# Optimization experiments

Hardware: AMD Instinct MI355X
Metric: run time of the kernel (lower is better)

## Reference

```python
import jax, jax.numpy as jnp
import numpy as np
import math

D = 768
H = 12
DH = D // H
L = 2
EPS = 1e-12
NEG = -10000.0


def layer_norm(x, w, b):
    u = jnp.mean(x, axis=-1, keepdims=True)
    s = jnp.mean((x - u) ** 2, axis=-1, keepdims=True)
    return w * ((x - u) / jnp.sqrt(s + EPS)) + b


def mha(q_in, k_in, v_in, mask, qw, qb, kw, kb, vw, vb):
    # q_in: (B,Lq,D); k_in/v_in: (B,Lk,D); mask: (B,Lq,Lk) or (B,1,Lk)
    B, Lq, _ = q_in.shape
    def proj(x, w, b):
        y = x @ w.T + b
        return y.reshape(x.shape[0], x.shape[1], H, DH).transpose(0, 2, 1, 3)
    q = proj(q_in, qw, qb)  # (B,H,Lq,DH)
    k = proj(k_in, kw, kb)
    v = proj(v_in, vw, vb)
    scores = jnp.einsum('bhqd,bhkd->bhqk', q, k) / math.sqrt(DH)
    scores = scores + (1.0 - mask[:, None]) * NEG  # additive mask, (B,1,Lq,Lk) broadcast
    probs = jax.nn.softmax(scores, axis=-1)
    ctx = jnp.einsum('bhqk,bhkd->bhqd', probs, v)
    return ctx.transpose(0, 2, 1, 3).reshape(B, Lq, D)


def setup_inputs() -> dict:
    key = jax.random.key(0)
    ks = jax.random.split(key, 8)
    B, Lt, Lv = 8, 1024, 512
    inp = {
        'dec_hidden_states': jax.random.normal(ks[0], (B, Lt, D), jnp.float32),
        'dec_mask': jnp.ones((B, Lt), jnp.float32),
        'enc_outputs': jax.random.normal(ks[1], (B, Lv, D), jnp.float32),
        'enc_mask': jnp.ones((B, Lv), jnp.float32),
    }
    wkeys = jax.random.split(ks[2], 7)
    names = ['sa_qw', 'sa_kw', 'sa_vw', 'ca_qw', 'ca_kw', 'ca_vw', 'out_w']
    for n, k in zip(names, wkeys):
        inp[n] = 0.02 * jax.random.normal(k, (L, D, D), jnp.float32)
    for n in ['sa_qb', 'sa_kb', 'sa_vb', 'ca_qb', 'ca_kb', 'ca_vb', 'out_b', 'n1_b', 'n2_b', 'n3_b']:
        inp[n] = jnp.zeros((L, D), jnp.float32)
    for n in ['n1_w', 'n2_w', 'n3_w']:
        inp[n] = jnp.ones((L, D), jnp.float32)
    return inp


def reference(dec_hidden_states, dec_mask, enc_outputs, enc_mask,
              sa_qw, sa_qb, sa_kw, sa_kb, sa_vw, sa_vb, n1_w, n1_b,
              ca_qw, ca_qb, ca_kw, ca_kb, ca_vw, ca_vb, n2_w, n2_b,
              out_w, out_b, n3_w, n3_b):
    Lt = dec_hidden_states.shape[1]
    causal = jnp.tril(jnp.ones((Lt, Lt), dec_mask.dtype))
    self_mask = dec_mask[:, None, :] * causal[None]        # (B,Lt,Lt)
    cross_mask = enc_mask[:, None, :]                      # (B,1,Lv)

    params = (sa_qw, sa_qb, sa_kw, sa_kb, sa_vw, sa_vb, n1_w, n1_b,
              ca_qw, ca_qb, ca_kw, ca_kb, ca_vw, ca_vb, n2_w, n2_b,
              out_w, out_b, n3_w, n3_b)

    def body(x, p):
        (qw, qb, kw, kb, vw, vb, w1, b1,
         cqw, cqb, ckw, ckb, cvw, cvb, w2, b2,
         ow, ob, w3, b3) = p
        a = mha(x, x, x, self_mask, qw, qb, kw, kb, vw, vb)
        x1 = layer_norm(a + x, w1, b1)
        c = mha(x1, enc_outputs, enc_outputs, cross_mask, cqw, cqb, ckw, ckb, cvw, cvb)
        x2 = layer_norm(x1 + c, w2, b2)
        # BertOutput called with (x2, x2): LN(dense(x2) + x2)
        y = layer_norm(x2 @ ow.T + ob + x2, w3, b3)
        return y, None

    out, _ = jax.lax.scan(body, dec_hidden_states, params)
    return out
```

## Files before the change

### kernel.cpp

```cpp
#include <hip/hip_runtime.h>
#include <hip/hip_bf16.h>

#define DMODEL 768
#define NH 12
#define DH 64
#define NEGC -10000.0f

#define AS1 __attribute__((address_space(1)))
#define AS3 __attribute__((address_space(3)))

typedef __bf16 bf16_t;
typedef __bf16 bf16x8 __attribute__((ext_vector_type(8)));
typedef float f32x4 __attribute__((ext_vector_type(4)));

__device__ __forceinline__ f32x4 mfma16(bf16x8 a, bf16x8 b, f32x4 c) {
    return __builtin_amdgcn_mfma_f32_16x16x32_bf16(a, b, c, 0, 0, 0);
}

__device__ __forceinline__ void gl_lds16(const bf16_t* g, void* l) {
    __builtin_amdgcn_global_load_lds((const AS1 void*)g, (AS3 void*)l, 16, 0, 0);
}

__global__ void probe_kernel(const unsigned int* m, int* flag) {
    *flag = (m[0] == 0x3F803F80u) ? 1 : 0;
}

__device__ __forceinline__ void cvt_group(const void* src, bf16_t* dst, int g, int isbf16) {
    if (isbf16) {
        ((bf16x8*)dst)[g] = ((const bf16x8*)src)[g];
    } else {
        const float* s = (const float*)src + (size_t)g * 8;
        bf16x8 v;
#pragma unroll
        for (int i = 0; i < 8; i++) v[i] = (bf16_t)s[i];
        ((bf16x8*)dst)[g] = v;
    }
}

__global__ __launch_bounds__(256) void cvt_kernel(const void* src, bf16_t* dst,
                                                  const int* flag, int n) {
    int g = blockIdx.x * 256 + threadIdx.x;
    if (g * 8 >= n) return;
    cvt_group(src, dst, g, *flag);
}

__global__ __launch_bounds__(256) void cvt7_kernel(
    const void* s0, const void* s1, const void* s2, const void* s3,
    const void* s4, const void* s5, const void* s6,
    bf16_t* dst, const int* flag)
{
    const void* srcs[7] = {s0, s1, s2, s3, s4, s5, s6};
    const void* src = srcs[blockIdx.y];
    bf16_t* d = dst + (size_t)blockIdx.y * 1179648;
    int g = blockIdx.x * 256 + threadIdx.x;
    cvt_group(src, d, g, *flag);
}

__global__ __launch_bounds__(256) void cvt13_kernel(
    const void* s0, const void* s1, const void* s2, const void* s3,
    const void* s4, const void* s5, const void* s6, const void* s7,
    const void* s8, const void* s9, const void* s10, const void* s11,
    const void* s12, bf16_t* dst, const int* flag)
{
    const void* srcs[13] = {s0, s1, s2, s3, s4, s5, s6, s7, s8, s9, s10, s11, s12};
    const void* src = srcs[blockIdx.x];
    bf16_t* d = dst + (size_t)blockIdx.x * 1536;
    int g = threadIdx.x;
    if (g >= 192) return;
    cvt_group(src, d, g, *flag);
}

__global__ __launch_bounds__(256) void gemm128_kernel(
    const bf16_t* __restrict__ X,
    const bf16_t* __restrict__ W0, const bf16_t* __restrict__ W1,
    const bf16_t* __restrict__ W2,
    const bf16_t* __restrict__ B0, const bf16_t* __restrict__ B1,
    const bf16_t* __restrict__ B2,
    bf16_t* __restrict__ O0, bf16_t* __restrict__ O1, bf16_t* __restrict__ O2,
    int nx, int ny, int nz, int vz, int lkShift)
{
    __shared__ __attribute__((aligned(16))) bf16_t alds[2][128 * 64];
    __shared__ __attribute__((aligned(16))) bf16_t blds[2][128 * 64];

    const int tid  = threadIdx.x;
    const int lane = tid & 63;
    const int w    = tid >> 6;
    const int r    = lane & 15;
    const int q4   = lane >> 4;

    const int id     = blockIdx.x;
    const int xcd    = id & 7;
    const int slot   = id >> 3;
    const int planes = nx * nz;
    const int band   = xcd + 8 * (slot / planes);
    const int p      = slot % planes;
    const int z      = p / nx;
    const int bx     = p - z * nx;
    const int row0   = band * 128;
    const int col0   = bx * 128;
    const int wrow   = (w >> 1) * 64;
    const int wcol   = (w & 1) * 64;

    const bf16_t* W    = (z == 0) ? W0 : ((z == 1) ? W1 : W2);
    const bf16_t* bias = (z == 0) ? B0 : ((z == 1) ? B1 : B2);
    bf16_t*       out  = (z == 0) ? O0 : ((z == 1) ? O1 : O2);
    const int     mode = (z == vz) ? 1 : 0;

    const f32x4 zero4 = {0.f, 0.f, 0.f, 0.f};
    f32x4 acc[4][4];
#pragma unroll
    for (int i = 0; i < 4; i++)
#pragma unroll
        for (int j = 0; j < 4; j++) acc[i][j] = zero4;

    const int srow = (w * 256 + lane) >> 3;
    const int sgc  = (lane & 7) ^ (srow & 7);
    const bf16_t* Xs = X + (size_t)(row0 + srow) * DMODEL + sgc * 8;
    const bf16_t* Ws = W + (size_t)(col0 + srow) * DMODEL + sgc * 8;

    auto stage = [&](int buf, int kb) {
#pragma unroll
        for (int j = 0; j < 4; j++) {
            gl_lds16(Xs + (size_t)(j * 8) * DMODEL + kb,
                     (char*)&alds[buf][0] + w * 4096 + j * 1024);
            gl_lds16(Ws + (size_t)(j * 8) * DMODEL + kb,
                     (char*)&blds[buf][0] + w * 4096 + j * 1024);
        }
    };

    const int NIT = DMODEL / 64;
    stage(0, 0);
    for (int i = 0; i < NIT; i++) {
        const int cur = i & 1;
        asm volatile("s_waitcnt lgkmcnt(0)" ::: "memory");
        __builtin_amdgcn_s_barrier();
        if (i + 1 < NIT) {
            stage(cur ^ 1, (i + 1) * 64);
            asm volatile("s_waitcnt vmcnt(8)" ::: "memory");
        } else {
            asm volatile("s_waitcnt vmcnt(0)" ::: "memory");
        }
        __builtin_amdgcn_s_barrier();

        const bf16_t* al = alds[cur];
        const bf16_t* bl = blds[cur];
#pragma unroll
        for (int ks = 0; ks < 2; ks++) {
            bf16x8 af[4], bf[4];
#pragma unroll
            for (int ii = 0; ii < 4; ii++) {
                int rr_ = wrow + ii * 16 + r;
                int pc  = (ks * 4 + q4) ^ (rr_ & 7);
                af[ii] = *(const bf16x8*)&al[rr_ * 64 + pc * 8];
            }
#pragma unroll
            for (int j = 0; j < 4; j++) {
                int cc_ = wcol + j * 16 + r;
                int pc  = (ks * 4 + q4) ^ (cc_ & 7);
                bf[j] = *(const bf16x8*)&bl[cc_ * 64 + pc * 8];
            }
#pragma unroll
            for (int ii = 0; ii < 4; ii++)
#pragma unroll
                for (int j = 0; j < 4; j++)
                    acc[ii][j] = mfma16(af[ii], bf[j], acc[ii][j]);
        }
    }

#pragma unroll
    for (int i = 0; i < 4; i++)
#pragma unroll
        for (int j = 0; j < 4; j++)
#pragma unroll
            for (int rr = 0; rr < 4; rr++) {
                int grow = row0 + wrow + i * 16 + q4 * 4 + rr;
                int gcol = col0 + wcol + j * 16 + r;
                float v = acc[i][j][rr] + (float)bias[gcol];
                if (mode == 0) {
                    out[(size_t)grow * DMODEL + gcol] = (bf16_t)v;
                } else {
                    int bidx = grow >> lkShift;
                    int t    = grow & ((1 << lkShift) - 1);
                    int h    = gcol >> 6;
                    int dd   = gcol & 63;
                    out[((size_t)((bidx * NH + h) * 64 + dd) << lkShift) + t] = (bf16_t)v;
                }
            }
}

__global__ __launch_bounds__(256) void attn_kernel(
    const bf16_t* Q, const bf16_t* __restrict__ K,
    const bf16_t* __restrict__ Vt, const bf16_t* __restrict__ mask,
    bf16_t* ctx, int Lq, int Lk, int causal)
{
    __shared__ __attribute__((aligned(16))) bf16_t kvlds[2][2][4096];
    __shared__ __attribute__((aligned(16))) bf16_t plds[4][1024];
    const int tid  = threadIdx.x;
    const int lane = tid & 63;
    const int wv   = tid >> 6;
    const int r    = lane & 15;
    const int q4   = lane >> 4;
    const int b    = blockIdx.z;
    const int h    = blockIdx.y;
    const int qblk = (gridDim.x - 1 - blockIdx.x) * 64;
    const int qbase = qblk + wv * 16;

    const bf16_t* Qp = Q + ((size_t)(b * Lq + qbase + r)) * DMODEL + h * DH + q4 * 8;
    bf16x8 qf0 = *(const bf16x8*)(Qp);
    bf16x8 qf1 = *(const bf16x8*)(Qp + 32);
    const bf16_t* Kg = K + ((size_t)b * Lk) * DMODEL + h * DH;
    const bf16_t* Vg = Vt + ((size_t)(b * NH + h) * DH) * Lk;
    const bf16_t* mp = mask + (size_t)b * Lk;

    const f32x4 zero4 = {0.f, 0.f, 0.f, 0.f};
    float psum[4] = {0.f, 0.f, 0.f, 0.f};
    f32x4 o[4] = {zero4, zero4, zero4, zero4};

    const int nt = causal ? ((qblk >> 6) + 1) : (Lk >> 6);

    auto stage = [&](int buf, int kb) {
#pragma unroll
        for (int j = 0; j < 2; j++) {
            gl_lds16(Kg + (size_t)(kb + wv * 16 + r) * DMODEL + (j * 4 + q4) * 8,
                     &kvlds[buf][0][wv * 1024 + j * 512]);
            gl_lds16(Vg + (size_t)(wv * 16 + r) * Lk + kb + (j * 4 + q4) * 8,
                     &kvlds[buf][1][wv * 1024 + j * 512]);
        }
    };

    stage(0, 0);
    for (int i = 0; i < nt; i++) {
        const int kb  = i << 6;
        const int cur = i & 1;
        asm volatile("s_waitcnt lgkmcnt(0)" ::: "memory");
        __builtin_amdgcn_s_barrier();
        float mb[4];
#pragma unroll
        for (int t = 0; t < 4; t++)
            mb[t] = (1.f - (float)mp[kb + t * 16 + r]) * NEGC;
        if (i + 1 < nt) {
            stage(cur ^ 1, kb + 64);
            asm volatile("s_waitcnt vmcnt(4)" ::: "memory");
        } else {
            asm volatile("s_waitcnt vmcnt(0)" ::: "memory");
        }
        __builtin_amdgcn_s_barrier();

        const bf16_t* kl = kvlds[cur][0];
        const bf16_t* vl = kvlds[cur][1];
        f32x4 s[4];
#pragma unroll
        for (int t = 0; t < 4; t++) {
            bf16x8 k0 = *(const bf16x8*)&kl[t * 1024 + lane * 8];
            bf16x8 k1 = *(const bf16x8*)&kl[t * 1024 + 512 + lane * 8];
            s[t] = mfma16(qf1, k1, mfma16(qf0, k0, zero4));
        }
#pragma unroll
        for (int t = 0; t < 4; t++) {
#pragma unroll
            for (int rr = 0; rr < 4; rr++) {
                float f = s[t][rr] * 0.125f + mb[t];
                float pv = __expf(f);
                if (causal && kb + t * 16 + r > qbase + q4 * 4 + rr) pv = 0.f;
                psum[rr] += pv;
                plds[wv][(t * 2 + (r >> 3)) * 128 + (q4 * 4 + rr) * 8 + (r & 7)] =
                    (bf16_t)pv;
            }
        }
        bf16x8 pa0 = *(const bf16x8*)&plds[wv][lane * 8];
        bf16x8 pa1 = *(const bf16x8*)&plds[wv][512 + lane * 8];
#pragma unroll
        for (int nc = 0; nc < 4; nc++) {
            bf16x8 v0 = *(const bf16x8*)&vl[nc * 1024 + lane * 8];
            bf16x8 v1 = *(const bf16x8*)&vl[nc * 1024 + 512 + lane * 8];
            o[nc] = mfma16(pa1, v1, mfma16(pa0, v0, o[nc]));
        }
    }

#pragma unroll
    for (int rr = 0; rr < 4; rr++) {
        psum[rr] += __shfl_xor(psum[rr], 1, 64);
        psum[rr] += __shfl_xor(psum[rr], 2, 64);
        psum[rr] += __shfl_xor(psum[rr], 4, 64);
        psum[rr] += __shfl_xor(psum[rr], 8, 64);
    }
#pragma unroll
    for (int nc = 0; nc < 4; nc++)
#pragma unroll
        for (int rr = 0; rr < 4; rr++) {
            int qi = qbase + q4 * 4 + rr;
            ctx[((size_t)(b * Lq + qi)) * DMODEL + h * DH + nc * 16 + r] =
                (bf16_t)(o[nc][rr] / psum[rr]);
        }
}

__global__ __launch_bounds__(256) void ln_kernel(
    const bf16_t* a, const bf16_t* res,
    const bf16_t* __restrict__ w, const bf16_t* __restrict__ b,
    void* out, int fin, const int* __restrict__ flag)
{
    __shared__ float red[8];
    const int row = blockIdx.x;
    const int tid = threadIdx.x;
    const int lane = tid & 63;
    const int wv = tid >> 6;
    const bf16_t* ap = a + (size_t)row * DMODEL;
    const bf16_t* rp = res + (size_t)row * DMODEL;
    const int outf32 = fin && (*flag == 0);

    float v[3];
#pragma unroll
    for (int i = 0; i < 3; i++) {
        int c = tid + i * 256;
        v[i] = (float)ap[c] + (float)rp[c];
    }
    float s = v[0] + v[1] + v[2];
#pragma unroll
    for (int m = 1; m < 64; m <<= 1) s += __shfl_xor(s, m, 64);
    if (lane == 0) red[wv] = s;
    __syncthreads();
    float u = (red[0] + red[1] + red[2] + red[3]) * (1.0f / DMODEL);
    float d0 = v[0] - u, d1 = v[1] - u, d2 = v[2] - u;
    float s2 = d0 * d0 + d1 * d1 + d2 * d2;
#pragma unroll
    for (int m = 1; m < 64; m <<= 1) s2 += __shfl_xor(s2, m, 64);
    if (lane == 0) red[4 + wv] = s2;
    __syncthreads();
    float var = (red[4] + red[5] + red[6] + red[7]) * (1.0f / DMODEL);
    float rstd = rsqrtf(var + 1e-12f);
#pragma unroll
    for (int i = 0; i < 3; i++) {
        int c = tid + i * 256;
        float y = ((v[i] - u) * rstd) * (float)w[c] + (float)b[c];
        if (outf32) ((float*)out)[(size_t)row * DMODEL + c] = y;
        else        ((bf16_t*)out)[(size_t)row * DMODEL + c] = (bf16_t)y;
    }
}

extern "C" void kernel_launch(void* const* d_in, const int* in_sizes, int n_in,
                              void* d_out, int out_size, void* d_ws, size_t ws_size,
                              hipStream_t stream)
{
    const int B = 8, Lt = 1024, Lv = 512;
    const size_t A = (size_t)B * Lt * DMODEL;
    const size_t E = (size_t)B * Lv * DMODEL;
    const size_t WT = 2 * (size_t)DMODEL * DMODEL;
    const int WSZ = DMODEL * DMODEL;

    char* p = (char*)d_ws;
    int* flagp = (int*)p;            p += 64;
    bf16_t* cdec = (bf16_t*)p;       p += A * 2;
    bf16_t* cenc = (bf16_t*)p;       p += E * 2;
    bf16_t* cdm  = (bf16_t*)p;       p += (size_t)B * Lt * 2;
    bf16_t* cem  = (bf16_t*)p;       p += (size_t)B * Lv * 2;
    bf16_t* cw   = (bf16_t*)p;       p += 7 * WT * 2;
    bf16_t* cb   = (bf16_t*)p;       p += 13 * 1536 * 2;
    bf16_t* b0   = (bf16_t*)p;       p += A * 2;
    bf16_t* b1   = (bf16_t*)p;       p += A * 2;
    bf16_t* b2   = (bf16_t*)p;       p += A * 2;
    bf16_t* dob  = (bf16_t*)d_out;

    const bf16_t* sa_qw = cw + 0 * WT, * sa_kw = cw + 1 * WT, * sa_vw = cw + 2 * WT;
    const bf16_t* ca_qw = cw + 3 * WT, * ca_kw = cw + 4 * WT, * ca_vw = cw + 5 * WT;
    const bf16_t* out_w = cw + 6 * WT;
    const bf16_t* sa_qb = cb + 0 * 1536, * sa_kb = cb + 1 * 1536, * sa_vb = cb + 2 * 1536;
    const bf16_t* ca_qb = cb + 3 * 1536, * ca_kb = cb + 4 * 1536, * ca_vb = cb + 5 * 1536;
    const bf16_t* out_b = cb + 6 * 1536;
    const bf16_t* n1_b  = cb + 7 * 1536, * n2_b = cb + 8 * 1536, * n3_b = cb + 9 * 1536;
    const bf16_t* n1_w  = cb + 10 * 1536, * n2_w = cb + 11 * 1536, * n3_w = cb + 12 * 1536;

    probe_kernel<<<1, 1, 0, stream>>>((const unsigned int*)d_in[1], flagp);
    cvt_kernel<<<dim3((unsigned)(A / 2048)), 256, 0, stream>>>(d_in[0], cdec, flagp, (int)A);
    cvt_kernel<<<dim3((unsigned)(E / 2048)), 256, 0, stream>>>(d_in[2], cenc, flagp, (int)E);
    cvt_kernel<<<dim3(4),  256, 0, stream>>>(d_in[1], cdm, flagp, B * Lt);
    cvt_kernel<<<dim3(2),  256, 0, stream>>>(d_in[3], cem, flagp, B * Lv);
    cvt7_kernel<<<dim3(576, 7), 256, 0, stream>>>(
        d_in[4], d_in[5], d_in[6], d_in[7], d_in[8], d_in[9], d_in[10], cw, flagp);
    cvt13_kernel<<<dim3(13), 256, 0, stream>>>(
        d_in[11], d_in[12], d_in[13], d_in[14], d_in[15], d_in[16], d_in[17],
        d_in[18], d_in[19], d_in[20], d_in[21], d_in[22], d_in[23], cb, flagp);

    const int Mdec = B * Lt;
    const int Menc = B * Lv;
    dim3 blk(256);
    dim3 gQKV(6 * 64 * 3);
    dim3 gOne(6 * 64 * 1);
    dim3 gKVe(6 * 32 * 2);
    dim3 gAttn(Lt / 64, NH, B);
    dim3 gLN(Mdec);

    for (int l = 0; l < 2; l++) {
        const bf16_t* xin = (l == 0) ? cdec : dob;
        gemm128_kernel<<<gQKV, blk, 0, stream>>>(
            xin, sa_qw + l * WSZ, sa_kw + l * WSZ, sa_vw + l * WSZ,
            sa_qb + l * DMODEL, sa_kb + l * DMODEL, sa_vb + l * DMODEL,
            b0, b1, b2, 6, 64, 3, 2, 10);
        attn_kernel<<<gAttn, blk, 0, stream>>>(b0, b1, b2, cdm, b0, Lt, Lt, 1);
        ln_kernel<<<gLN, blk, 0, stream>>>(b0, xin, n1_w + l * DMODEL, n1_b + l * DMODEL, b0, 0, flagp);
        gemm128_kernel<<<gOne, blk, 0, stream>>>(
            b0, ca_qw + l * WSZ, ca_qw, ca_qw,
            ca_qb + l * DMODEL, ca_qb, ca_qb,
            b1, b1, b1, 6, 64, 1, -1, 0);
        gemm128_kernel<<<gKVe, blk, 0, stream>>>(
            cenc, ca_kw + l * WSZ, ca_vw + l * WSZ, ca_vw,
            ca_kb + l * DMODEL, ca_vb + l * DMODEL, ca_vb,
            b2, dob, dob, 6, 32, 2, 1, 9);
        attn_kernel<<<gAttn, blk, 0, stream>>>(b1, b2, dob, cem, b1, Lt, Lv, 0);
        ln_kernel<<<gLN, blk, 0, stream>>>(b1, b0, n2_w + l * DMODEL, n2_b + l * DMODEL, b1, 0, flagp);
        gemm128_kernel<<<gOne, blk, 0, stream>>>(
            b1, out_w + l * WSZ, out_w, out_w,
            out_b + l * DMODEL, out_b, out_b,
            b2, b2, b2, 6, 64, 1, -1, 0);
        ln_kernel<<<gLN, blk, 0, stream>>>(b2, b1, n3_w + l * DMODEL, n3_b + l * DMODEL, dob, (l == 1) ? 1 : 0, flagp);
    }
}
```

Before: 702.7 us.

## Halve GEMM K-tile to raise occupancy and merge cross-attn Q/KV launches

The GEMM's LDS K-tile drops from 64 to 32, halving shared memory per block, and launch bounds now request 4 blocks per CU to increase occupancy. The swizzle and staging are adjusted to match, and the loop runs twice as many iterations. The GEMM now takes a separate input pointer and row-band count per z-plane, so the cross-attention Q projection (decoder rows) and the K/V projections (encoder rows) run in one launch, with excess blocks exiting early. This cuts one launch and lets the smaller GEMMs share the device, at the cost of more barriers per K step and idle early-exit blocks.

Result: no change. 697.7 us (-0.7%).

```diff
diff --git a/kernel.cpp b/kernel.cpp
--- a/kernel.cpp
+++ b/kernel.cpp
@@ -70,17 +70,18 @@
     cvt_group(src, d, g, *flag);
 }
 
-__global__ __launch_bounds__(256) void gemm128_kernel(
-    const bf16_t* __restrict__ X,
+__global__ __launch_bounds__(256, 4) void gemm128_kernel(
+    const bf16_t* __restrict__ X0, const bf16_t* __restrict__ X1,
+    const bf16_t* __restrict__ X2,
     const bf16_t* __restrict__ W0, const bf16_t* __restrict__ W1,
     const bf16_t* __restrict__ W2,
     const bf16_t* __restrict__ B0, const bf16_t* __restrict__ B1,
     const bf16_t* __restrict__ B2,
     bf16_t* __restrict__ O0, bf16_t* __restrict__ O1, bf16_t* __restrict__ O2,
-    int nx, int ny, int nz, int vz, int lkShift)
-{
-    __shared__ __attribute__((aligned(16))) bf16_t alds[2][128 * 64];
-    __shared__ __attribute__((aligned(16))) bf16_t blds[2][128 * 64];
+    int nx, int ny0, int ny1, int ny2, int nz, int vz, int lkShift)
+{
+    __shared__ __attribute__((aligned(16))) bf16_t alds[2][128 * 32];
+    __shared__ __attribute__((aligned(16))) bf16_t blds[2][128 * 32];
 
     const int tid  = threadIdx.x;
     const int lane = tid & 63;
@@ -96,11 +97,16 @@
     const int p      = slot % planes;
     const int z      = p / nx;
     const int bx     = p - z * nx;
+
+    const int nyz = (z == 0) ? ny0 : ((z == 1) ? ny1 : ny2);
+    if (band >= nyz) return;
+
     const int row0   = band * 128;
     const int col0   = bx * 128;
     const int wrow   = (w >> 1) * 64;
     const int wcol   = (w & 1) * 64;
 
+    const bf16_t* X    = (z == 0) ? X0 : ((z == 1) ? X1 : X2);
     const bf16_t* W    = (z == 0) ? W0 : ((z == 1) ? W1 : W2);
     const bf16_t* bias = (z == 0) ? B0 : ((z == 1) ? B1 : B2);
     bf16_t*       out  = (z == 0) ? O0 : ((z == 1) ? O1 : O2);
@@ -113,30 +119,30 @@
 #pragma unroll
         for (int j = 0; j < 4; j++) acc[i][j] = zero4;
 
-    const int srow = (w * 256 + lane) >> 3;
-    const int sgc  = (lane & 7) ^ (srow & 7);
+    const int srow = w * 32 + (lane >> 2);
+    const int sgc  = (lane & 3) ^ (srow & 3);
     const bf16_t* Xs = X + (size_t)(row0 + srow) * DMODEL + sgc * 8;
     const bf16_t* Ws = W + (size_t)(col0 + srow) * DMODEL + sgc * 8;
 
     auto stage = [&](int buf, int kb) {
 #pragma unroll
-        for (int j = 0; j < 4; j++) {
-            gl_lds16(Xs + (size_t)(j * 8) * DMODEL + kb,
-                     (char*)&alds[buf][0] + w * 4096 + j * 1024);
-            gl_lds16(Ws + (size_t)(j * 8) * DMODEL + kb,
-                     (char*)&blds[buf][0] + w * 4096 + j * 1024);
+        for (int j = 0; j < 2; j++) {
+            gl_lds16(Xs + (size_t)(j * 16) * DMODEL + kb,
+                     (char*)&alds[buf][0] + w * 2048 + j * 1024);
+            gl_lds16(Ws + (size_t)(j * 16) * DMODEL + kb,
+                     (char*)&blds[buf][0] + w * 2048 + j * 1024);
         }
     };
 
-    const int NIT = DMODEL / 64;
+    const int NIT = DMODEL / 32;
     stage(0, 0);
     for (int i = 0; i < NIT; i++) {
         const int cur = i & 1;
         asm volatile("s_waitcnt lgkmcnt(0)" ::: "memory");
         __builtin_amdgcn_s_barrier();
         if (i + 1 < NIT) {
-            stage(cur ^ 1, (i + 1) * 64);
-            asm volatile("s_waitcnt vmcnt(8)" ::: "memory");
+            stage(cur ^ 1, (i + 1) * 32);
+            asm volatile("s_waitcnt vmcnt(4)" ::: "memory");
         } else {
             asm volatile("s_waitcnt vmcnt(0)" ::: "memory");
         }
@@ -144,27 +150,24 @@
 
         const bf16_t* al = alds[cur];
         const bf16_t* bl = blds[cur];
-#pragma unroll
-        for (int ks = 0; ks < 2; ks++) {
-            bf16x8 af[4], bf[4];
-#pragma unroll
-            for (int ii = 0; ii < 4; ii++) {
-                int rr_ = wrow + ii * 16 + r;
-                int pc  = (ks * 4 + q4) ^ (rr_ & 7);
-                af[ii] = *(const bf16x8*)&al[rr_ * 64 + pc * 8];
-            }
-#pragma unroll
-            for (int j = 0; j < 4; j++) {
-                int cc_ = wcol + j * 16 + r;
-                int pc  = (ks * 4 + q4) ^ (cc_ & 7);
-                bf[j] = *(const bf16x8*)&bl[cc_ * 64 + pc * 8];
-            }
-#pragma unroll
-            for (int ii = 0; ii < 4; ii++)
-#pragma unroll
-                for (int j = 0; j < 4; j++)
-                    acc[ii][j] = mfma16(af[ii], bf[j], acc[ii][j]);
-        }
+        bf16x8 af[4], bf[4];
+#pragma unroll
+        for (int ii = 0; ii < 4; ii++) {
+            int rr_ = wrow + ii * 16 + r;
+            int pc  = q4 ^ (rr_ & 3);
+            af[ii] = *(const bf16x8*)&al[rr_ * 32 + pc * 8];
+        }
+#pragma unroll
+        for (int j = 0; j < 4; j++) {
+            int cc_ = wcol + j * 16 + r;
+            int pc  = q4 ^ (cc_ & 3);
+            bf[j] = *(const bf16x8*)&bl[cc_ * 32 + pc * 8];
+        }
+#pragma unroll
+        for (int ii = 0; ii < 4; ii++)
+#pragma unroll
+            for (int j = 0; j < 4; j++)
+                acc[ii][j] = mfma16(af[ii], bf[j], acc[ii][j]);
     }
 
 #pragma unroll
@@ -380,37 +383,34 @@
         d_in[11], d_in[12], d_in[13], d_in[14], d_in[15], d_in[16], d_in[17],
         d_in[18], d_in[19], d_in[20], d_in[21], d_in[22], d_in[23], cb, flagp);
 
-    const int Mdec = B * Lt;
-    const int Menc = B * Lv;
     dim3 blk(256);
     dim3 gQKV(6 * 64 * 3);
+    dim3 gCrs(6 * 64 * 3);
     dim3 gOne(6 * 64 * 1);
-    dim3 gKVe(6 * 32 * 2);
     dim3 gAttn(Lt / 64, NH, B);
-    dim3 gLN(Mdec);
+    dim3 gLN(B * Lt);
 
     for (int l = 0; l < 2; l++) {
         const bf16_t* xin = (l == 0) ? cdec : dob;
         gemm128_kernel<<<gQKV, blk, 0, stream>>>(
-            xin, sa_qw + l * WSZ, sa_kw + l * WSZ, sa_vw + l * WSZ,
+            xin, xin, xin,
+            sa_qw + l * WSZ, sa_kw + l * WSZ, sa_vw + l * WSZ,
             sa_qb + l * DMODEL, sa_kb + l * DMODEL, sa_vb + l * DMODEL,
-            b0, b1, b2, 6, 64, 3, 2, 10);
+            b0, b1, b2, 6, 64, 64, 64, 3, 2, 10);
         attn_kernel<<<gAttn, blk, 0, stream>>>(b0, b1, b2, cdm, b0, Lt, Lt, 1);
         ln_kernel<<<gLN, blk, 0, stream>>>(b0, xin, n1_w + l * DMODEL, n1_b + l * DMODEL, b0, 0, flagp);
-        gemm128_kernel<<<gOne, blk, 0, stream>>>(
-            b0, ca_qw + l * WSZ, ca_qw, ca_qw,
-            ca_qb + l * DMODEL, ca_qb, ca_qb,
-            b1, b1, b1, 6, 64, 1, -1, 0);
-        gemm128_kernel<<<gKVe, blk, 0, stream>>>(
-            cenc, ca_kw + l * WSZ, ca_vw + l * WSZ, ca_vw,
-            ca_kb + l * DMODEL, ca_vb + l * DMODEL, ca_vb,
-            b2, dob, dob, 6, 32, 2, 1, 9);
+        gemm128_kernel<<<gCrs, blk, 0, stream>>>(
+            b0, cenc, cenc,
+            ca_qw + l * WSZ, ca_kw + l * WSZ, ca_vw + l * WSZ,
+            ca_qb + l * DMODEL, ca_kb + l * DMODEL, ca_vb + l * DMODEL,
+            b1, b2, dob, 6, 64, 32, 32, 3, 2, 9);
         attn_kernel<<<gAttn, blk, 0, stream>>>(b1, b2, dob, cem, b1, Lt, Lv, 0);
         ln_kernel<<<gLN, blk, 0, stream>>>(b1, b0, n2_w + l * DMODEL, n2_b + l * DMODEL, b1, 0, flagp);
         gemm128_kernel<<<gOne, blk, 0, stream>>>(
-            b1, out_w + l * WSZ, out_w, out_w,
+            b1, b1, b1,
+            out_w + l * WSZ, out_w, out_w,
             out_b + l * DMODEL, out_b, out_b,
-            b2, b2, b2, 6, 64, 1, -1, 0);
+            b2, b2, b2, 6, 64, 64, 64, 1, -1, 0);
         ln_kernel<<<gLN, blk, 0, stream>>>(b2, b1, n3_w + l * DMODEL, n3_b + l * DMODEL, dob, (l == 1) ? 1 : 0, flagp);
     }
 }
```

## Use 256x256-tile GEMM for QKV projections and merge cross-attention Q/KV launches

Applied to the files above, without the earlier changes.

Adds a 512-thread GEMM kernel with 256x256 output tiles and per-plane input pointers, used for the self-attention QKV projection and the cross-attention projections. The cross-attention Q projection (from decoder states) and K/V projections (from encoder outputs) now run in one launch, with bands beyond each plane's row count exiting early. The transposed V output is written as packed 4-element vector stores. Larger tiles raise operand reuse and cut launches, but the grid shrinks to 288 blocks with large LDS use, which risks partial-wave imbalance and lower occupancy on the device.

New measurement: 672.8 us. -4.3%, faster.

```diff
diff --git a/kernel.cpp b/kernel.cpp
--- a/kernel.cpp
+++ b/kernel.cpp
@@ -12,6 +12,7 @@
 typedef __bf16 bf16_t;
 typedef __bf16 bf16x8 __attribute__((ext_vector_type(8)));
 typedef float f32x4 __attribute__((ext_vector_type(4)));
+typedef unsigned int u32x2 __attribute__((ext_vector_type(2)));
 
 __device__ __forceinline__ f32x4 mfma16(bf16x8 a, bf16x8 b, f32x4 c) {
     return __builtin_amdgcn_mfma_f32_16x16x32_bf16(a, b, c, 0, 0, 0);
@@ -70,17 +71,18 @@
     cvt_group(src, d, g, *flag);
 }
 
-__global__ __launch_bounds__(256) void gemm128_kernel(
-    const bf16_t* __restrict__ X,
+__global__ __launch_bounds__(512, 2) void gemm256_kernel(
+    const bf16_t* __restrict__ X0, const bf16_t* __restrict__ X1,
+    const bf16_t* __restrict__ X2,
     const bf16_t* __restrict__ W0, const bf16_t* __restrict__ W1,
     const bf16_t* __restrict__ W2,
     const bf16_t* __restrict__ B0, const bf16_t* __restrict__ B1,
     const bf16_t* __restrict__ B2,
     bf16_t* __restrict__ O0, bf16_t* __restrict__ O1, bf16_t* __restrict__ O2,
-    int nx, int ny, int nz, int vz, int lkShift)
-{
-    __shared__ __attribute__((aligned(16))) bf16_t alds[2][128 * 64];
-    __shared__ __attribute__((aligned(16))) bf16_t blds[2][128 * 64];
+    int nx, int ny0, int ny1, int ny2, int nz, int vz, int lkShift)
+{
+    __shared__ __attribute__((aligned(16))) bf16_t alds[2][256 * 64];
+    __shared__ __attribute__((aligned(16))) bf16_t blds[2][256 * 64];
 
     const int tid  = threadIdx.x;
     const int lane = tid & 63;
@@ -96,24 +98,31 @@
     const int p      = slot % planes;
     const int z      = p / nx;
     const int bx     = p - z * nx;
-    const int row0   = band * 128;
-    const int col0   = bx * 128;
-    const int wrow   = (w >> 1) * 64;
-    const int wcol   = (w & 1) * 64;
-
+
+    const int nyz = (z == 0) ? ny0 : ((z == 1) ? ny1 : ny2);
+    if (band >= nyz) return;
+
+    const int row0 = band * 256;
+    const int col0 = bx * 256;
+    const int wr   = w >> 2;
+    const int wc   = w & 3;
+    const int wrow = wr * 128;
+    const int wcol = wc * 64;
+
+    const bf16_t* X    = (z == 0) ? X0 : ((z == 1) ? X1 : X2);
     const bf16_t* W    = (z == 0) ? W0 : ((z == 1) ? W1 : W2);
     const bf16_t* bias = (z == 0) ? B0 : ((z == 1) ? B1 : B2);
     bf16_t*       out  = (z == 0) ? O0 : ((z == 1) ? O1 : O2);
     const int     mode = (z == vz) ? 1 : 0;
 
     const f32x4 zero4 = {0.f, 0.f, 0.f, 0.f};
-    f32x4 acc[4][4];
-#pragma unroll
-    for (int i = 0; i < 4; i++)
+    f32x4 acc[8][4];
+#pragma unroll
+    for (int i = 0; i < 8; i++)
 #pragma unroll
         for (int j = 0; j < 4; j++) acc[i][j] = zero4;
 
-    const int srow = (w * 256 + lane) >> 3;
+    const int srow = w * 32 + (lane >> 3);
     const int sgc  = (lane & 7) ^ (srow & 7);
     const bf16_t* Xs = X + (size_t)(row0 + srow) * DMODEL + sgc * 8;
     const bf16_t* Ws = W + (size_t)(col0 + srow) * DMODEL + sgc * 8;
@@ -146,6 +155,121 @@
         const bf16_t* bl = blds[cur];
 #pragma unroll
         for (int ks = 0; ks < 2; ks++) {
+            bf16x8 af[8], bf[4];
+#pragma unroll
+            for (int ii = 0; ii < 8; ii++) {
+                int rr_ = wrow + ii * 16 + r;
+                int pc  = (ks * 4 + q4) ^ (rr_ & 7);
+                af[ii] = *(const bf16x8*)&al[rr_ * 64 + pc * 8];
+            }
+#pragma unroll
+            for (int j = 0; j < 4; j++) {
+                int cc_ = wcol + j * 16 + r;
+                int pc  = (ks * 4 + q4) ^ (cc_ & 7);
+                bf[j] = *(const bf16x8*)&bl[cc_ * 64 + pc * 8];
+            }
+#pragma unroll
+            for (int ii = 0; ii < 8; ii++)
+#pragma unroll
+                for (int j = 0; j < 4; j++)
+                    acc[ii][j] = mfma16(af[ii], bf[j], acc[ii][j]);
+        }
+    }
+
+#pragma unroll
+    for (int i = 0; i < 8; i++)
+#pragma unroll
+        for (int j = 0; j < 4; j++) {
+            int gcol = col0 + wcol + j * 16 + r;
+            float bv = (float)bias[gcol];
+            if (mode == 0) {
+#pragma unroll
+                for (int rr = 0; rr < 4; rr++) {
+                    int grow = row0 + wrow + i * 16 + q4 * 4 + rr;
+                    out[(size_t)grow * DMODEL + gcol] = (bf16_t)(acc[i][j][rr] + bv);
+                }
+            } else {
+                int growb = row0 + wrow + i * 16 + q4 * 4;
+                int bidx  = growb >> lkShift;
+                int t     = growb & ((1 << lkShift) - 1);
+                int h     = gcol >> 6;
+                int dd    = gcol & 63;
+                union { bf16_t h4[4]; u32x2 v; } pk;
+#pragma unroll
+                for (int rr = 0; rr < 4; rr++)
+                    pk.h4[rr] = (bf16_t)(acc[i][j][rr] + bv);
+                *reinterpret_cast<u32x2*>(
+                    &out[((size_t)((bidx * NH + h) * 64 + dd) << lkShift) + t]) = pk.v;
+            }
+        }
+}
+
+__global__ __launch_bounds__(256) void gemm128_kernel(
+    const bf16_t* __restrict__ X,
+    const bf16_t* __restrict__ W,
+    const bf16_t* __restrict__ Bb,
+    bf16_t* __restrict__ out,
+    int nx, int ny)
+{
+    __shared__ __attribute__((aligned(16))) bf16_t alds[2][128 * 64];
+    __shared__ __attribute__((aligned(16))) bf16_t blds[2][128 * 64];
+
+    const int tid  = threadIdx.x;
+    const int lane = tid & 63;
+    const int w    = tid >> 6;
+    const int r    = lane & 15;
+    const int q4   = lane >> 4;
+
+    const int id     = blockIdx.x;
+    const int xcd    = id & 7;
+    const int slot   = id >> 3;
+    const int band   = xcd + 8 * (slot / nx);
+    const int bx     = slot % nx;
+    const int row0   = band * 128;
+    const int col0   = bx * 128;
+    const int wrow   = (w >> 1) * 64;
+    const int wcol   = (w & 1) * 64;
+
+    const f32x4 zero4 = {0.f, 0.f, 0.f, 0.f};
+    f32x4 acc[4][4];
+#pragma unroll
+    for (int i = 0; i < 4; i++)
+#pragma unroll
+        for (int j = 0; j < 4; j++) acc[i][j] = zero4;
+
+    const int srow = w * 32 + (lane >> 3);
+    const int sgc  = (lane & 7) ^ (srow & 7);
+    const bf16_t* Xs = X + (size_t)(row0 + srow) * DMODEL + sgc * 8;
+    const bf16_t* Ws = W + (size_t)(col0 + srow) * DMODEL + sgc * 8;
+
+    auto stage = [&](int buf, int kb) {
+#pragma unroll
+        for (int j = 0; j < 4; j++) {
+            gl_lds16(Xs + (size_t)(j * 8) * DMODEL + kb,
+                     (char*)&alds[buf][0] + w * 4096 + j * 1024);
+            gl_lds16(Ws + (size_t)(j * 8) * DMODEL + kb,
+                     (char*)&blds[buf][0] + w * 4096 + j * 1024);
+        }
+    };
+
+    const int NIT = DMODEL / 64;
+    stage(0, 0);
+    for (int i = 0; i < NIT; i++) {
+        const int cur = i & 1;
+        asm volatile("s_waitcnt lgkmcnt(0)" ::: "memory");
+        __builtin_amdgcn_s_barrier();
+        if (i + 1 < NIT) {
+            stage(cur ^ 1, (i + 1) * 64);
+            asm volatile("s_waitcnt vmcnt(8)" ::: "memory");
+        } else {
+            asm volatile("s_waitcnt vmcnt(0)" ::: "memory");
+        }
+        __builtin_amdgcn_s_barrier();
+
+        const bf16_t* al = alds[cur];
+        const bf16_t* bl = blds[cur];
+#pragma unroll
+        for (int ks = 0; ks < 2; ks++) {
             bf16x8 af[4], bf[4];
 #pragma unroll
             for (int ii = 0; ii < 4; ii++) {
@@ -170,22 +294,15 @@
 #pragma unroll
     for (int i = 0; i < 4; i++)
 #pragma unroll
-        for (int j = 0; j < 4; j++)
+        for (int j = 0; j < 4; j++) {
+            int gcol = col0 + wcol + j * 16 + r;
+            float bv = (float)Bb[gcol];
 #pragma unroll
             for (int rr = 0; rr < 4; rr++) {
                 int grow = row0 + wrow + i * 16 + q4 * 4 + rr;
-                int gcol = col0 + wcol + j * 16 + r;
-                float v = acc[i][j][rr] + (float)bias[gcol];
-                if (mode == 0) {
-                    out[(size_t)grow * DMODEL + gcol] = (bf16_t)v;
-                } else {
-                    int bidx = grow >> lkShift;
-                    int t    = grow & ((1 << lkShift) - 1);
-                    int h    = gcol >> 6;
-                    int dd   = gcol & 63;
-                    out[((size_t)((bidx * NH + h) * 64 + dd) << lkShift) + t] = (bf16_t)v;
-                }
-            }
+                out[(size_t)grow * DMODEL + gcol] = (bf16_t)(acc[i][j][rr] + bv);
+            }
+        }
 }
 
 __global__ __launch_bounds__(256) void attn_kernel(
@@ -380,37 +497,32 @@
         d_in[11], d_in[12], d_in[13], d_in[14], d_in[15], d_in[16], d_in[17],
         d_in[18], d_in[19], d_in[20], d_in[21], d_in[22], d_in[23], cb, flagp);
 
-    const int Mdec = B * Lt;
-    const int Menc = B * Lv;
-    dim3 blk(256);
-    dim3 gQKV(6 * 64 * 3);
-    dim3 gOne(6 * 64 * 1);
-    dim3 gKVe(6 * 32 * 2);
+    dim3 blk256(256);
+    dim3 blk512(512);
+    dim3 gQKV(3 * 32 * 3);
+    dim3 gCrs(3 * 32 * 3);
+    dim3 gOne(6 * 64);
     dim3 gAttn(Lt / 64, NH, B);
-    dim3 gLN(Mdec);
+    dim3 gLN(B * Lt);
 
     for (int l = 0; l < 2; l++) {
         const bf16_t* xin = (l == 0) ? cdec : dob;
-        gemm128_kernel<<<gQKV, blk, 0, stream>>>(
-            xin, sa_qw + l * WSZ, sa_kw + l * WSZ, sa_vw + l * WSZ,
+        gemm256_kernel<<<gQKV, blk512, 0, stream>>>(
+            xin, xin, xin,
+            sa_qw + l * WSZ, sa_kw + l * WSZ, sa_vw + l * WSZ,
             sa_qb + l * DMODEL, sa_kb + l * DMODEL, sa_vb + l * DMODEL,
-            b0, b1, b2, 6, 64, 3, 2, 10);
-        attn_kernel<<<gAttn, blk, 0, stream>>>(b0, b1, b2, cdm, b0, Lt, Lt, 1);
-        ln_kernel<<<gLN, blk, 0, stream>>>(b0, xin, n1_w + l * DMODEL, n1_b + l * DMODEL, b0, 0, flagp);
-        gemm128_kernel<<<gOne, blk, 0, stream>>>(
-            b0, ca_qw + l * WSZ, ca_qw, ca_qw,
-            ca_qb + l * DMODEL, ca_qb, ca_qb,
-            b1, b1, b1, 6, 64, 1, -1, 0);
-        gemm128_kernel<<<gKVe, blk, 0, stream>>>(
-            cenc, ca_kw + l * WSZ, ca_vw + l * WSZ, ca_vw,
-            ca_kb + l * DMODEL, ca_vb + l * DMODEL, ca_vb,
-            b2, dob, dob, 6, 32, 2, 1, 9);
-        attn_kernel<<<gAttn, blk, 0, stream>>>(b1, b2, dob, cem, b1, Lt, Lv, 0);
-        ln_kernel<<<gLN, blk, 0, stream>>>(b1, b0, n2_w + l * DMODEL, n2_b + l * DMODEL, b1, 0, flagp);
-        gemm128_kernel<<<gOne, blk, 0, stream>>>(
-            b1, out_w + l * WSZ, out_w, out_w,
-            out_b + l * DMODEL, out_b, out_b,
-            b2, b2, b2, 6, 64, 1, -1, 0);
-        ln_kernel<<<gLN, blk, 0, stream>>>(b2, b1, n3_w + l * DMODEL, n3_b + l * DMODEL, dob, (l == 1) ? 1 : 0, flagp);
-    }
-}
+            b0, b1, b2, 3, 32, 32, 32, 3, 2, 10);
+        attn_kernel<<<gAttn, blk256, 0, stream>>>(b0, b1, b2, cdm, b0, Lt, Lt, 1);
+        ln_kernel<<<gLN, blk256, 0, stream>>>(b0, xin, n1_w + l * DMODEL, n1_b + l * DMODEL, b0, 0, flagp);
+        gemm256_kernel<<<gCrs, blk512, 0, stream>>>(
+            b0, cenc, cenc,
+            ca_qw + l * WSZ, ca_kw + l * WSZ, ca_vw + l * WSZ,
+            ca_qb + l * DMODEL, ca_kb + l * DMODEL, ca_vb + l * DMODEL,
+            b1, b2, dob, 3, 32, 16, 16, 3, 2, 9);
+        attn_kernel<<<gAttn, blk256, 0, stream>>>(b1, b2, dob, cem, b1, Lt, Lv, 0);
+        ln_kernel<<<gLN, blk256, 0, stream>>>(b1, b0, n2_w + l * DMODEL, n2_b + l * DMODEL, b1, 0, flagp);
+        gemm128_kernel<<<gOne, blk256, 0, stream>>>(
+            b1, out_w + l * WSZ, out_b + l * DMODEL, b2, 6, 64);
+        ln_kernel<<<gLN, blk256, 0, stream>>>(b2, b1, n3_w + l * DMODEL, n3_b + l * DMODEL, dob, (l == 1) ? 1 : 0, flagp);
+    }
+}
```
